# Kernel tuning notes

Measured on AMD Instinct MI355X. Metric: run time of the kernel, lower is better.

## Reference

```python
import jax, jax.numpy as jnp
import numpy as np

N = 100000   # nodes
E = 1600000  # edges
IN, H1, H2, OUT = 128, 256, 128, 16


def setup_inputs() -> dict:
    key = jax.random.key(0)
    ks = jax.random.split(key, 20)

    def lin(kw, fan_in, fan_out):
        s = 1.0 / np.sqrt(fan_in)
        return jax.random.uniform(kw, (fan_in, fan_out), jnp.float32, -s, s)

    inp = {
        "x": jax.random.normal(ks[0], (N, IN), jnp.float32),
        "edge_index": jax.random.randint(ks[1], (2, E), 0, N, jnp.int64),
        # main branch
        "W1": lin(ks[2], IN, H1), "b1": jnp.zeros((H1,), jnp.float32),
        "W2": lin(ks[3], H1, H2), "b2": jnp.zeros((H2,), jnp.float32),
        "Wc": lin(ks[4], H2, OUT), "bc": jnp.zeros((OUT,), jnp.float32),
        # encoder branch (4 GCN layers)
        "We1": lin(ks[5], IN, H2), "be1": jnp.zeros((H2,), jnp.float32),
        "We2": lin(ks[6], H2, H2), "be2": jnp.zeros((H2,), jnp.float32),
        "We3": lin(ks[7], H2, H2), "be3": jnp.zeros((H2,), jnp.float32),
        "We4": lin(ks[8], H2, H2), "be4": jnp.zeros((H2,), jnp.float32),
        # trustworthiness head
        "Wt": lin(ks[9], H2, 2), "bt": jnp.zeros((2,), jnp.float32),
    }
    return inp


def _gcn(x, W, b, row, col, dis):
    # PyG GCNConv: out = D^-1/2 (A + I) D^-1/2 (x W) + b
    xw = x @ W                                   # [N, F]
    norm = dis[row] * dis[col]                   # [E]
    msg = xw[row] * norm[:, None]                # [E, F]  (gather + scale)
    agg = jax.ops.segment_sum(msg, col, num_segments=N)
    agg = agg + xw * (dis * dis)[:, None]        # self-loop contribution
    return agg + b


def reference(x, edge_index, W1, b1, W2, b2, Wc, bc,
              We1, be1, We2, be2, We3, be3, We4, be4, Wt, bt):
    row, col = edge_index[0], edge_index[1]
    # degree with self-loops, shared across all conv layers (same graph)
    deg = jax.ops.segment_sum(jnp.ones((E,), x.dtype), col, num_segments=N) + 1.0
    dis = deg ** -0.5

    # classification branch
    h = jax.nn.relu(_gcn(x, W1, b1, row, col, dis))
    h = _gcn(h, W2, b2, row, col, dis)
    class_logits = h @ Wc + bc

    # encoder branch -> trust head
    h2 = _gcn(x, We1, be1, row, col, dis)
    h2 = _gcn(h2, We2, be2, row, col, dis)
    h2 = _gcn(h2, We3, be3, row, col, dis)
    h2 = _gcn(h2, We4, be4, row, col, dis)
    trust_prob = jax.nn.sigmoid(h2 @ Wt + bt)

    return (class_logits, trust_prob)
```

## Files before the change

kernel.cpp:

```cpp
#include <hip/hip_runtime.h>
#include <math.h>


#define SM_W2C   0
#define SM_T4    4096
#define SM_T3    4352
#define SM_T2    4608
#define SM_ME    4864
#define SM_CLSC  5120
#define SM_C1    5136
#define SM_C2    5138
#define SM_C3    5140
#define SM_FC    5142
#define SM_TOTAL 5248

typedef __attribute__((ext_vector_type(8))) short bf16x8;
typedef __attribute__((ext_vector_type(4))) float f32x4;
#define MFMA16(a, b, c) __builtin_amdgcn_mfma_f32_16x16x32_bf16(a, b, c, 0, 0, 0)

__device__ inline unsigned short f2bf(float f) {
  unsigned u = __float_as_uint(f);
  u += 0x7fffu + ((u >> 16) & 1u);
  return (unsigned short)(u >> 16);
}
__device__ inline float bf2f(unsigned short h) {
  return __uint_as_float((unsigned)h << 16);
}

__global__ __launch_bounds__(256) void k_deg(const int* __restrict__ ei,
                                             int* __restrict__ deg, int E, int N) {
  int e = blockIdx.x * 256 + threadIdx.x;
  if (e < E) {
    unsigned c = (unsigned)ei[E + e];
    if (c >= (unsigned)N) c = 0;
    atomicAdd(&deg[c], 1);
  }
}

__global__ __launch_bounds__(1024) void k_scan1(const int* __restrict__ deg,
                                                int* __restrict__ rowptr,
                                                int* __restrict__ bsum,
                                                float* __restrict__ dis, int n) {
  __shared__ int wsum[16];
  int tid = threadIdx.x, lane = tid & 63, wid = tid >> 6;
  int i = blockIdx.x * 1024 + tid;
  int v = (i < n) ? deg[i] : 0;
  if (i < n) dis[i] = 1.0f / sqrtf((float)v + 1.0f);
  int x = v;
  #pragma unroll
  for (int off = 1; off < 64; off <<= 1) {
    int t = __shfl_up(x, off, 64);
    if (lane >= off) x += t;
  }
  if (lane == 63) wsum[wid] = x;
  __syncthreads();
  if (wid == 0 && lane < 16) {
    int ws = wsum[lane];
    #pragma unroll
    for (int off = 1; off < 16; off <<= 1) {
      int t = __shfl_up(ws, off, 64);
      if (lane >= off) ws += t;
    }
    wsum[lane] = ws;
  }
  __syncthreads();
  int incl = x + (wid ? wsum[wid - 1] : 0);
  if (i < n) rowptr[i + 1] = incl;
  if (tid == 0) bsum[blockIdx.x] = wsum[15];
}

__global__ __launch_bounds__(128) void k_scan2(int* __restrict__ bsum,
                                               int* __restrict__ rowptr, int B) {
  __shared__ int s[128];
  int tid = threadIdx.x;
  s[tid] = (tid < B) ? bsum[tid] : 0;
  __syncthreads();
  if (tid == 0) {
    int acc = 0;
    for (int j = 0; j < B; ++j) { int t = s[j]; s[j] = acc; acc += t; }
    rowptr[0] = 0;
  }
  __syncthreads();
  if (tid < B) bsum[tid] = s[tid];
}

__global__ __launch_bounds__(256) void k_scan3(int* __restrict__ rowptr,
                                               const int* __restrict__ bsum, int n) {
  int i = blockIdx.x * 256 + threadIdx.x;
  if (i < n) rowptr[i + 1] += bsum[i >> 10];
}

__global__ __launch_bounds__(256) void k_scatter(const int* __restrict__ ei,
                                                 const int* __restrict__ rowptr,
                                                 int* __restrict__ cnt,
                                                 const float* __restrict__ dis,
                                                 int* __restrict__ csr_src,
                                                 float* __restrict__ csr_w,
                                                 int E, int N) {
  int e = blockIdx.x * 256 + threadIdx.x;
  if (e >= E) return;
  unsigned r = (unsigned)ei[e];
  unsigned c = (unsigned)ei[E + e];
  if (r >= (unsigned)N) r = 0;
  if (c >= (unsigned)N) c = 0;
  int pos = rowptr[c] + atomicAdd(&cnt[c], 1);
  csr_src[pos] = (int)r;
  csr_w[pos] = dis[r] * dis[c];
}

__global__ __launch_bounds__(256) void k_precompute(
    const float* __restrict__ W1,
    const float* __restrict__ W2, const float* __restrict__ b2,
    const float* __restrict__ Wc, const float* __restrict__ bc,
    const float* __restrict__ We1, const float* __restrict__ be1,
    const float* __restrict__ We2, const float* __restrict__ be2,
    const float* __restrict__ We3, const float* __restrict__ be3,
    const float* __restrict__ We4, const float* __restrict__ be4,
    const float* __restrict__ Wt, const float* __restrict__ bt,
    float* __restrict__ sm,
    unsigned short* __restrict__ w1h, unsigned short* __restrict__ w1l,
    unsigned short* __restrict__ w2h, unsigned short* __restrict__ w2l) {
  int tid = threadIdx.x, b = blockIdx.x;
  if (b < 16) {
    int r = b * 16 + (tid >> 4), c = tid & 15;
    float s = 0.f;
    #pragma unroll 4
    for (int k = 0; k < 128; ++k) s += W2[(size_t)r * 128 + k] * Wc[k * 16 + c];
    sm[SM_W2C + r * 16 + c] = s;
    unsigned short h = f2bf(s);
    w2h[c * 256 + r] = h;
    w2l[c * 256 + r] = f2bf(s - bf2f(h));
    return;
  }
  if (b < 32) {
    int base = (b - 16) * 2048;
    #pragma unroll
    for (int it = 0; it < 8; ++it) {
      int idx = base + it * 256 + tid;
      int c = idx >> 7, k = idx & 127;
      float v = W1[(size_t)k * 256 + c];
      unsigned short h = f2bf(v);
      w1h[idx] = h;
      w1l[idx] = f2bf(v - bf2f(h));
    }
    return;
  }
  {
    int r = tid >> 1, c = tid & 1; float s = 0.f;
    for (int k = 0; k < 128; ++k) s += We4[r * 128 + k] * Wt[k * 2 + c];
    sm[SM_T4 + r * 2 + c] = s;
  }
  __syncthreads();
  {
    int r = tid >> 1, c = tid & 1; float s = 0.f;
    for (int k = 0; k < 128; ++k) s += We3[r * 128 + k] * sm[SM_T4 + k * 2 + c];
    sm[SM_T3 + r * 2 + c] = s;
  }
  __syncthreads();
  {
    int r = tid >> 1, c = tid & 1; float s = 0.f;
    for (int k = 0; k < 128; ++k) s += We2[r * 128 + k] * sm[SM_T3 + k * 2 + c];
    sm[SM_T2 + r * 2 + c] = s;
  }
  __syncthreads();
  {
    int r = tid >> 1, c = tid & 1; float s = 0.f;
    for (int k = 0; k < 128; ++k) s += We1[r * 128 + k] * sm[SM_T2 + k * 2 + c];
    sm[SM_ME + r * 2 + c] = s;
  }
  if (tid < 16) {
    float s = 0.f;
    for (int k = 0; k < 128; ++k) s += b2[k] * Wc[k * 16 + tid];
    sm[SM_CLSC + tid] = s + bc[tid];
  }
  __syncthreads();
  if (tid < 2) {
    float s = 0.f;
    for (int k = 0; k < 128; ++k) s += be1[k] * sm[SM_T2 + k * 2 + tid];
    sm[SM_C1 + tid] = s;
    s = 0.f;
    for (int k = 0; k < 128; ++k) s += be2[k] * sm[SM_T3 + k * 2 + tid];
    sm[SM_C2 + tid] = s;
    s = 0.f;
    for (int k = 0; k < 128; ++k) s += be3[k] * sm[SM_T4 + k * 2 + tid];
    sm[SM_C3 + tid] = s;
    s = 0.f;
    for (int k = 0; k < 128; ++k) s += be4[k] * Wt[k * 2 + tid];
    sm[SM_FC + tid] = s + bt[tid];
  }
}

__global__ __launch_bounds__(256) void k_agg128(
    const float* __restrict__ x, const int* __restrict__ rowptr,
    const int* __restrict__ csr_src, const float* __restrict__ csr_w,
    const float* __restrict__ dis, const float* __restrict__ sm,
    unsigned short* __restrict__ axh, unsigned short* __restrict__ axl,
    float* __restrict__ ga, int N) {
  int node = blockIdx.x * 4 + (threadIdx.x >> 6);
  if (node >= N) return;
  int lane = threadIdx.x & 63;
  const float2* x2 = (const float2*)x;
  float d = dis[node];
  float2 v = x2[(size_t)node * 64 + lane];
  float a0 = d * d * v.x, a1 = d * d * v.y;
  int e = rowptr[node], end = rowptr[node + 1];
  while (e < end) {
    int rem = end - e;
    int cnt = rem < 64 ? rem : 64;
    int off = lane < cnt ? lane : cnt - 1;
    int src_l = csr_src[e + off];
    int w_l = __float_as_int(csr_w[e + off]);
    for (int i = 0; i < cnt; ++i) {
      int s = __builtin_amdgcn_readlane(src_l, i);
      float w = __int_as_float(__builtin_amdgcn_readlane(w_l, i));
      float2 u = x2[(size_t)s * 64 + lane];
      a0 = fmaf(w, u.x, a0);
      a1 = fmaf(w, u.y, a1);
    }
    e += 64;
  }
  unsigned short h0 = f2bf(a0), h1v = f2bf(a1);
  unsigned short l0 = f2bf(a0 - bf2f(h0)), l1 = f2bf(a1 - bf2f(h1v));
  ((unsigned int*)axh)[(size_t)node * 64 + lane] = (unsigned)h0 | ((unsigned)h1v << 16);
  ((unsigned int*)axl)[(size_t)node * 64 + lane] = (unsigned)l0 | ((unsigned)l1 << 16);
  float4 me = *(const float4*)&sm[SM_ME + lane * 4];
  float p0 = a0 * me.x + a1 * me.z;
  float p1 = a0 * me.y + a1 * me.w;
  #pragma unroll
  for (int m = 32; m; m >>= 1) { p0 += __shfl_xor(p0, m); p1 += __shfl_xor(p1, m); }
  if (lane == 0)
    ((float2*)ga)[node] = make_float2(p0 + sm[SM_C1 + 0], p1 + sm[SM_C1 + 1]);
}

__global__ __launch_bounds__(256, 2) void k_gemm_mfma(
    const unsigned short* __restrict__ axh, const unsigned short* __restrict__ axl,
    const unsigned short* __restrict__ w1h, const unsigned short* __restrict__ w1l,
    const unsigned short* __restrict__ w2h, const unsigned short* __restrict__ w2l,
    const float* __restrict__ b1, float* __restrict__ Y, int N) {
  __shared__ unsigned short lds[32768];
  int tid = threadIdx.x, lane = tid & 63, w = tid >> 6;
  int r16 = lane & 15, kh = lane >> 4;
  int m0 = blockIdx.x * 64;
  #pragma unroll
  for (int it = 0; it < 8; ++it) {
    int idx = it * 256 + tid;
    int arr = idx >> 10, rem = idx & 1023;
    int row = rem >> 4, ch = rem & 15;
    int gr = m0 + row; if (gr > N - 1) gr = N - 1;
    const unsigned short* src = (arr ? axl : axh) + (size_t)gr * 128 + ch * 8;
    uint4 vv = *(const uint4*)src;
    *(uint4*)&lds[arr * 8192 + row * 128 + ((ch ^ (row & 7)) * 8)] = vv;
  }
  __syncthreads();
  f32x4 acc[4][4];
  #pragma unroll
  for (int i = 0; i < 4; ++i)
    #pragma unroll
    for (int j = 0; j < 4; ++j) acc[i][j] = (f32x4){0.f, 0.f, 0.f, 0.f};
  #pragma unroll
  for (int ks = 0; ks < 4; ++ks) {
    bf16x8 bh[4], bl[4];
    #pragma unroll
    for (int nt = 0; nt < 4; ++nt) {
      int col = w * 64 + nt * 16 + r16;
      size_t boff = (size_t)col * 128 + ks * 32 + kh * 8;
      bh[nt] = *(const bf16x8*)(w1h + boff);
      bl[nt] = *(const bf16x8*)(w1l + boff);
    }
    #pragma unroll
    for (int mt = 0; mt < 4; ++mt) {
      int row = mt * 16 + r16;
      int ch = ks * 4 + kh;
      int off = row * 128 + ((ch ^ (row & 7)) * 8);
      bf16x8 ah = *(const bf16x8*)&lds[off];
      bf16x8 al = *(const bf16x8*)&lds[8192 + off];
      #pragma unroll
      for (int nt = 0; nt < 4; ++nt) {
        acc[mt][nt] = MFMA16(ah, bh[nt], acc[mt][nt]);
        acc[mt][nt] = MFMA16(ah, bl[nt], acc[mt][nt]);
        acc[mt][nt] = MFMA16(al, bh[nt], acc[mt][nt]);
      }
    }
  }
  __syncthreads();
  #pragma unroll
  for (int nt = 0; nt < 4; ++nt) {
    int colL = w * 64 + nt * 16 + r16;
    float bv = b1[colL];
    #pragma unroll
    for (int mt = 0; mt < 4; ++mt) {
      #pragma unroll
      for (int r = 0; r < 4; ++r) {
        int rowL = mt * 16 + kh * 4 + r;
        float vv = acc[mt][nt][r] + bv;
        vv = vv > 0.f ? vv : 0.f;
        unsigned short hh = f2bf(vv);
        unsigned short ll = f2bf(vv - bf2f(hh));
        int idx = rowL * 256 + (colL ^ ((rowL & 7) << 3));
        lds[idx] = hh;
        lds[16384 + idx] = ll;
      }
    }
  }
  __syncthreads();
  f32x4 y = (f32x4){0.f, 0.f, 0.f, 0.f};
  int rowL = w * 16 + r16;
  #pragma unroll
  for (int k2 = 0; k2 < 8; ++k2) {
    int cb = k2 * 32 + kh * 8;
    int idx = rowL * 256 + (cb ^ ((rowL & 7) << 3));
    bf16x8 a2h = *(const bf16x8*)&lds[idx];
    bf16x8 a2l = *(const bf16x8*)&lds[16384 + idx];
    size_t boff = (size_t)r16 * 256 + cb;
    bf16x8 b2h = *(const bf16x8*)(w2h + boff);
    bf16x8 b2l = *(const bf16x8*)(w2l + boff);
    y = MFMA16(a2h, b2h, y);
    y = MFMA16(a2h, b2l, y);
    y = MFMA16(a2l, b2h, y);
  }
  #pragma unroll
  for (int r = 0; r < 4; ++r) {
    int gr = m0 + w * 16 + kh * 4 + r;
    if (gr < N) Y[(size_t)gr * 16 + r16] = y[r];
  }
}

__global__ __launch_bounds__(256) void k_agg16(
    const float* __restrict__ Y, const int* __restrict__ rowptr,
    const int* __restrict__ csr_src, const float* __restrict__ csr_w,
    const float* __restrict__ dis, const float* __restrict__ sm,
    float* __restrict__ out, int N) {
  int node = blockIdx.x * 16 + (threadIdx.x >> 4);
  if (node >= N) return;
  int sl = threadIdx.x & 15;
  float d = dis[node];
  float acc = d * d * Y[(size_t)node * 16 + sl];
  int e = rowptr[node], end = rowptr[node + 1];
  for (; e < end; ++e) {
    int s = csr_src[e]; float w = csr_w[e];
    acc = fmaf(w, Y[(size_t)s * 16 + sl], acc);
  }
  out[(size_t)node * 16 + sl] = acc + sm[SM_CLSC + sl];
}

template <int FINAL>
__global__ __launch_bounds__(256) void k_agg2(
    const float* __restrict__ gin, const int* __restrict__ rowptr,
    const int* __restrict__ csr_src, const float* __restrict__ csr_w,
    const float* __restrict__ dis, const float* __restrict__ cadd,
    float* __restrict__ gout, int N) {
  int i = blockIdx.x * 256 + threadIdx.x;
  if (i >= N) return;
  const float2* g2 = (const float2*)gin;
  float d = dis[i];
  float2 v = g2[i];
  float a0 = d * d * v.x, a1 = d * d * v.y;
  int e = rowptr[i], end = rowptr[i + 1];
  for (; e < end; ++e) {
    int s = csr_src[e]; float w = csr_w[e];
    float2 u = g2[s];
    a0 = fmaf(w, u.x, a0); a1 = fmaf(w, u.y, a1);
  }
  a0 += cadd[0]; a1 += cadd[1];
  if (FINAL) {
    a0 = 1.f / (1.f + expf(-a0));
    a1 = 1.f / (1.f + expf(-a1));
  }
  ((float2*)gout)[i] = make_float2(a0, a1);
}

extern "C" void kernel_launch(void* const* d_in, const int* in_sizes, int n_in,
                              void* d_out, int out_size, void* d_ws, size_t ws_size,
                              hipStream_t stream) {
  const float* x = (const float*)d_in[0];
  const int* ei = (const int*)d_in[1];
  const float* W1 = (const float*)d_in[2];
  const float* b1 = (const float*)d_in[3];
  const float* W2 = (const float*)d_in[4];
  const float* b2 = (const float*)d_in[5];
  const float* Wc = (const float*)d_in[6];
  const float* bc = (const float*)d_in[7];
  const float* We1 = (const float*)d_in[8];
  const float* be1 = (const float*)d_in[9];
  const float* We2 = (const float*)d_in[10];
  const float* be2 = (const float*)d_in[11];
  const float* We3 = (const float*)d_in[12];
  const float* be3 = (const float*)d_in[13];
  const float* We4 = (const float*)d_in[14];
  const float* be4 = (const float*)d_in[15];
  const float* Wt = (const float*)d_in[16];
  const float* bt = (const float*)d_in[17];
  float* out = (float*)d_out;

  const int N = in_sizes[0] / 128;
  const int E = in_sizes[1] / 2;
  const int NB = (N + 1023) / 1024;

  char* ws = (char*)d_ws;
  size_t off = 0;
  auto alloc = [&](size_t bytes) {
    size_t o = off;
    off = (off + bytes + 255) & ~(size_t)255;
    return o;
  };
  int* deg = (int*)(ws + alloc((size_t)N * 8));
  int* cnt = deg + N;
  int* rowptr = (int*)(ws + alloc(((size_t)N + 1) * 4));
  int* bsum = (int*)(ws + alloc(128 * 4));
  float* dis = (float*)(ws + alloc((size_t)N * 4));
  int* csr_src = (int*)(ws + alloc((size_t)E * 4));
  float* csr_w = (float*)(ws + alloc((size_t)E * 4));
  unsigned short* axh = (unsigned short*)(ws + alloc((size_t)N * 128 * 2));
  unsigned short* axl = (unsigned short*)(ws + alloc((size_t)N * 128 * 2));
  float* y16 = (float*)(ws + alloc((size_t)N * 16 * 4));
  float* ga = (float*)(ws + alloc((size_t)N * 2 * 4));
  float* gb = (float*)(ws + alloc((size_t)N * 2 * 4));
  float* sm = (float*)(ws + alloc((size_t)SM_TOTAL * 4));
  unsigned short* w1h = (unsigned short*)(ws + alloc(32768 * 2));
  unsigned short* w1l = (unsigned short*)(ws + alloc(32768 * 2));
  unsigned short* w2h = (unsigned short*)(ws + alloc(4096 * 2));
  unsigned short* w2l = (unsigned short*)(ws + alloc(4096 * 2));

  hipMemsetAsync(deg, 0, (size_t)N * 8, stream);

  k_precompute<<<33, 256, 0, stream>>>(W1, W2, b2, Wc, bc, We1, be1, We2, be2,
                                       We3, be3, We4, be4, Wt, bt, sm,
                                       w1h, w1l, w2h, w2l);
  k_deg<<<(E + 255) / 256, 256, 0, stream>>>(ei, deg, E, N);
  k_scan1<<<NB, 1024, 0, stream>>>(deg, rowptr, bsum, dis, N);
  k_scan2<<<1, 128, 0, stream>>>(bsum, rowptr, NB);
  k_scan3<<<(N + 255) / 256, 256, 0, stream>>>(rowptr, bsum, N);
  k_scatter<<<(E + 255) / 256, 256, 0, stream>>>(ei, rowptr, cnt, dis, csr_src,
                                                 csr_w, E, N);
  k_agg128<<<(N + 3) / 4, 256, 0, stream>>>(x, rowptr, csr_src, csr_w, dis, sm,
                                            axh, axl, ga, N);
  k_gemm_mfma<<<(N + 63) / 64, 256, 0, stream>>>(axh, axl, w1h, w1l, w2h, w2l,
                                                 b1, y16, N);
  k_agg16<<<(N + 15) / 16, 256, 0, stream>>>(y16, rowptr, csr_src, csr_w, dis,
                                             sm, out, N);
  k_agg2<0><<<(N + 255) / 256, 256, 0, stream>>>(ga, rowptr, csr_src, csr_w,
                                                 dis, sm + SM_C2, gb, N);
  k_agg2<0><<<(N + 255) / 256, 256, 0, stream>>>(gb, rowptr, csr_src, csr_w,
                                                 dis, sm + SM_C3, ga, N);
  k_agg2<1><<<(N + 255) / 256, 256, 0, stream>>>(
      ga, rowptr, csr_src, csr_w, dis, sm + SM_FC, out + (size_t)N * 16, N);
}
```

Baseline: 582.0 us.

## Drop per-edge weight array, factor normalization, fuse agg16 with first agg2

Removes the csr_w per-edge weight array. Each aggregation now weights neighbours by dis[src] and multiplies by dis[dst] once at the end, which also turns the self-loop term into d*x. The 16-wide class aggregation is fused with the first 2-wide encoder aggregation, so one kernel traverses the CSR for both and one launch disappears. cnt zeroing moves into the scan kernel, which halves the memset. The cost is an extra random gather of dis[src] per edge in exchange for not streaming csr_w, plus minor floating-point reassociation.

```diff
diff --git a/kernel.cpp b/kernel.cpp
--- a/kernel.cpp
+++ b/kernel.cpp
@@ -40,12 +40,16 @@
 __global__ __launch_bounds__(1024) void k_scan1(const int* __restrict__ deg,
                                                 int* __restrict__ rowptr,
                                                 int* __restrict__ bsum,
-                                                float* __restrict__ dis, int n) {
+                                                float* __restrict__ dis,
+                                                int* __restrict__ cnt, int n) {
   __shared__ int wsum[16];
   int tid = threadIdx.x, lane = tid & 63, wid = tid >> 6;
   int i = blockIdx.x * 1024 + tid;
   int v = (i < n) ? deg[i] : 0;
-  if (i < n) dis[i] = 1.0f / sqrtf((float)v + 1.0f);
+  if (i < n) {
+    dis[i] = 1.0f / sqrtf((float)v + 1.0f);
+    cnt[i] = 0;
+  }
   int x = v;
   #pragma unroll
   for (int off = 1; off < 64; off <<= 1) {
@@ -93,9 +97,7 @@
 __global__ __launch_bounds__(256) void k_scatter(const int* __restrict__ ei,
                                                  const int* __restrict__ rowptr,
                                                  int* __restrict__ cnt,
-                                                 const float* __restrict__ dis,
                                                  int* __restrict__ csr_src,
-                                                 float* __restrict__ csr_w,
                                                  int E, int N) {
   int e = blockIdx.x * 256 + threadIdx.x;
   if (e >= E) return;
@@ -105,7 +107,6 @@
   if (c >= (unsigned)N) c = 0;
   int pos = rowptr[c] + atomicAdd(&cnt[c], 1);
   csr_src[pos] = (int)r;
-  csr_w[pos] = dis[r] * dis[c];
 }
 
 __global__ __launch_bounds__(256) void k_precompute(
@@ -192,8 +193,8 @@
 
 __global__ __launch_bounds__(256) void k_agg128(
     const float* __restrict__ x, const int* __restrict__ rowptr,
-    const int* __restrict__ csr_src, const float* __restrict__ csr_w,
-    const float* __restrict__ dis, const float* __restrict__ sm,
+    const int* __restrict__ csr_src, const float* __restrict__ dis,
+    const float* __restrict__ sm,
     unsigned short* __restrict__ axh, unsigned short* __restrict__ axl,
     float* __restrict__ ga, int N) {
   int node = blockIdx.x * 4 + (threadIdx.x >> 6);
@@ -202,23 +203,24 @@
   const float2* x2 = (const float2*)x;
   float d = dis[node];
   float2 v = x2[(size_t)node * 64 + lane];
-  float a0 = d * d * v.x, a1 = d * d * v.y;
+  float a0 = d * v.x, a1 = d * v.y;
   int e = rowptr[node], end = rowptr[node + 1];
   while (e < end) {
     int rem = end - e;
     int cnt = rem < 64 ? rem : 64;
     int off = lane < cnt ? lane : cnt - 1;
     int src_l = csr_src[e + off];
-    int w_l = __float_as_int(csr_w[e + off]);
+    int wbits = __float_as_int(dis[src_l]);
     for (int i = 0; i < cnt; ++i) {
       int s = __builtin_amdgcn_readlane(src_l, i);
-      float w = __int_as_float(__builtin_amdgcn_readlane(w_l, i));
+      float w = __int_as_float(__builtin_amdgcn_readlane(wbits, i));
       float2 u = x2[(size_t)s * 64 + lane];
       a0 = fmaf(w, u.x, a0);
       a1 = fmaf(w, u.y, a1);
     }
     e += 64;
   }
+  a0 *= d; a1 *= d;
   unsigned short h0 = f2bf(a0), h1v = f2bf(a1);
   unsigned short l0 = f2bf(a0 - bf2f(h0)), l1 = f2bf(a1 - bf2f(h1v));
   ((unsigned int*)axh)[(size_t)node * 64 + lane] = (unsigned)h0 | ((unsigned)h1v << 16);
@@ -325,43 +327,53 @@
   }
 }
 
-__global__ __launch_bounds__(256) void k_agg16(
-    const float* __restrict__ Y, const int* __restrict__ rowptr,
-    const int* __restrict__ csr_src, const float* __restrict__ csr_w,
+__global__ __launch_bounds__(256) void k_agg18(
+    const float* __restrict__ Y, const float* __restrict__ g,
+    const int* __restrict__ rowptr, const int* __restrict__ csr_src,
     const float* __restrict__ dis, const float* __restrict__ sm,
-    float* __restrict__ out, int N) {
+    float* __restrict__ out, float* __restrict__ gout, int N) {
   int node = blockIdx.x * 16 + (threadIdx.x >> 4);
   if (node >= N) return;
   int sl = threadIdx.x & 15;
+  const float2* g2 = (const float2*)g;
   float d = dis[node];
-  float acc = d * d * Y[(size_t)node * 16 + sl];
+  float acc = d * Y[(size_t)node * 16 + sl];
+  float2 gv = g2[node];
+  float ga0 = d * gv.x, ga1 = d * gv.y;
   int e = rowptr[node], end = rowptr[node + 1];
   for (; e < end; ++e) {
-    int s = csr_src[e]; float w = csr_w[e];
+    int s = csr_src[e];
+    float w = dis[s];
     acc = fmaf(w, Y[(size_t)s * 16 + sl], acc);
-  }
-  out[(size_t)node * 16 + sl] = acc + sm[SM_CLSC + sl];
+    float2 gu = g2[s];
+    ga0 = fmaf(w, gu.x, ga0);
+    ga1 = fmaf(w, gu.y, ga1);
+  }
+  out[(size_t)node * 16 + sl] = d * acc + sm[SM_CLSC + sl];
+  if (sl == 0)
+    ((float2*)gout)[node] =
+        make_float2(d * ga0 + sm[SM_C2 + 0], d * ga1 + sm[SM_C2 + 1]);
 }
 
 template <int FINAL>
 __global__ __launch_bounds__(256) void k_agg2(
     const float* __restrict__ gin, const int* __restrict__ rowptr,
-    const int* __restrict__ csr_src, const float* __restrict__ csr_w,
-    const float* __restrict__ dis, const float* __restrict__ cadd,
-    float* __restrict__ gout, int N) {
+    const int* __restrict__ csr_src, const float* __restrict__ dis,
+    const float* __restrict__ cadd, float* __restrict__ gout, int N) {
   int i = blockIdx.x * 256 + threadIdx.x;
   if (i >= N) return;
   const float2* g2 = (const float2*)gin;
   float d = dis[i];
   float2 v = g2[i];
-  float a0 = d * d * v.x, a1 = d * d * v.y;
+  float a0 = d * v.x, a1 = d * v.y;
   int e = rowptr[i], end = rowptr[i + 1];
   for (; e < end; ++e) {
-    int s = csr_src[e]; float w = csr_w[e];
+    int s = csr_src[e];
+    float w = dis[s];
     float2 u = g2[s];
     a0 = fmaf(w, u.x, a0); a1 = fmaf(w, u.y, a1);
   }
-  a0 += cadd[0]; a1 += cadd[1];
+  a0 = d * a0 + cadd[0]; a1 = d * a1 + cadd[1];
   if (FINAL) {
     a0 = 1.f / (1.f + expf(-a0));
     a1 = 1.f / (1.f + expf(-a1));
@@ -403,13 +415,12 @@
     off = (off + bytes + 255) & ~(size_t)255;
     return o;
   };
-  int* deg = (int*)(ws + alloc((size_t)N * 8));
-  int* cnt = deg + N;
+  int* deg = (int*)(ws + alloc((size_t)N * 4));
+  int* cnt = (int*)(ws + alloc((size_t)N * 4));
   int* rowptr = (int*)(ws + alloc(((size_t)N + 1) * 4));
   int* bsum = (int*)(ws + alloc(128 * 4));
   float* dis = (float*)(ws + alloc((size_t)N * 4));
   int* csr_src = (int*)(ws + alloc((size_t)E * 4));
-  float* csr_w = (float*)(ws + alloc((size_t)E * 4));
   unsigned short* axh = (unsigned short*)(ws + alloc((size_t)N * 128 * 2));
   unsigned short* axl = (unsigned short*)(ws + alloc((size_t)N * 128 * 2));
   float* y16 = (float*)(ws + alloc((size_t)N * 16 * 4));
@@ -421,27 +432,24 @@
   unsigned short* w2h = (unsigned short*)(ws + alloc(4096 * 2));
   unsigned short* w2l = (unsigned short*)(ws + alloc(4096 * 2));
 
-  hipMemsetAsync(deg, 0, (size_t)N * 8, stream);
+  hipMemsetAsync(deg, 0, (size_t)N * 4, stream);
 
   k_precompute<<<33, 256, 0, stream>>>(W1, W2, b2, Wc, bc, We1, be1, We2, be2,
                                        We3, be3, We4, be4, Wt, bt, sm,
                                        w1h, w1l, w2h, w2l);
   k_deg<<<(E + 255) / 256, 256, 0, stream>>>(ei, deg, E, N);
-  k_scan1<<<NB, 1024, 0, stream>>>(deg, rowptr, bsum, dis, N);
+  k_scan1<<<NB, 1024, 0, stream>>>(deg, rowptr, bsum, dis, cnt, N);
   k_scan2<<<1, 128, 0, stream>>>(bsum, rowptr, NB);
   k_scan3<<<(N + 255) / 256, 256, 0, stream>>>(rowptr, bsum, N);
-  k_scatter<<<(E + 255) / 256, 256, 0, stream>>>(ei, rowptr, cnt, dis, csr_src,
-                                                 csr_w, E, N);
-  k_agg128<<<(N + 3) / 4, 256, 0, stream>>>(x, rowptr, csr_src, csr_w, dis, sm,
+  k_scatter<<<(E + 255) / 256, 256, 0, stream>>>(ei, rowptr, cnt, csr_src, E, N);
+  k_agg128<<<(N + 3) / 4, 256, 0, stream>>>(x, rowptr, csr_src, dis, sm,
                                             axh, axl, ga, N);
   k_gemm_mfma<<<(N + 63) / 64, 256, 0, stream>>>(axh, axl, w1h, w1l, w2h, w2l,
                                                  b1, y16, N);
-  k_agg16<<<(N + 15) / 16, 256, 0, stream>>>(y16, rowptr, csr_src, csr_w, dis,
-                                             sm, out, N);
-  k_agg2<0><<<(N + 255) / 256, 256, 0, stream>>>(ga, rowptr, csr_src, csr_w,
-                                                 dis, sm + SM_C2, gb, N);
-  k_agg2<0><<<(N + 255) / 256, 256, 0, stream>>>(gb, rowptr, csr_src, csr_w,
-                                                 dis, sm + SM_C3, ga, N);
+  k_agg18<<<(N + 15) / 16, 256, 0, stream>>>(y16, ga, rowptr, csr_src, dis, sm,
+                                             out, gb, N);
+  k_agg2<0><<<(N + 255) / 256, 256, 0, stream>>>(gb, rowptr, csr_src, dis,
+                                                 sm + SM_C3, ga, N);
   k_agg2<1><<<(N + 255) / 256, 256, 0, stream>>>(
-      ga, rowptr, csr_src, csr_w, dis, sm + SM_FC, out + (size_t)N * 16, N);
-}
+      ga, rowptr, csr_src, dis, sm + SM_FC, out + (size_t)N * 16, N);
+}
```

Result: slower. 601.0 us (+3.3%).
